# Kernel optimization log

Hardware: AMD Instinct MI355X
Metric: run time of the kernel (lower is better)

## Reference

```python
import jax, jax.numpy as jnp
from jax import lax
import numpy as np

NT, NGRID, NX = 365, 3000, 20
H, NY = 256, 1


def setup_inputs() -> dict:
    key = jax.random.key(0)
    ks = jax.random.split(key, 12)
    x = jax.random.normal(ks[0], (NT, NGRID, NX), dtype=jnp.float32)
    y = jax.random.normal(ks[1], (NT, NGRID, NY), dtype=jnp.float32)
    obs_mask = jax.random.bernoulli(ks[2], 0.7, (NT, NGRID, NY))
    y = jnp.where(obs_mask, y, jnp.nan)
    s_in = 1.0 / np.sqrt(NX + 1)
    s_h = 1.0 / np.sqrt(H)
    w_in = jax.random.uniform(ks[3], (H, NX + 1), jnp.float32, -s_in, s_in)
    b_in = jax.random.uniform(ks[4], (H,), jnp.float32, -s_in, s_in)
    w_ih = jax.random.uniform(ks[5], (4 * H, H), jnp.float32, -s_h, s_h)
    b_ih = jax.random.uniform(ks[6], (4 * H,), jnp.float32, -s_h, s_h)
    w_hh = jax.random.uniform(ks[7], (4 * H, H), jnp.float32, -s_h, s_h)
    b_hh = jax.random.uniform(ks[8], (4 * H,), jnp.float32, -s_h, s_h)
    w_out = jax.random.uniform(ks[9], (NY, H), jnp.float32, -s_h, s_h)
    b_out = jax.random.uniform(ks[10], (NY,), jnp.float32, -s_h, s_h)
    return {"x": x, "y": y, "w_in": w_in, "b_in": b_in, "w_ih": w_ih,
            "b_ih": b_ih, "w_hh": w_hh, "b_hh": b_hh, "w_out": w_out,
            "b_out": b_out}


def reference(x, y, w_in, b_in, w_ih, b_ih, w_hh, b_hh, w_out, b_out):
    nt, ngrid, nx = x.shape
    h0 = jnp.zeros((ngrid, H), x.dtype)
    c0 = jnp.zeros((ngrid, H), x.dtype)
    y0 = jnp.zeros((ngrid, NY), x.dtype)

    def step(carry, inp):
        h, c, yt = carry
        xt, yobs = inp                      # [ngrid,nx], [ngrid,ny]
        mask = ~jnp.isnan(yobs)
        yt = jnp.where(mask, yobs, yt)      # fill observed values
        xcat = jnp.concatenate([xt, yt], axis=1)          # [ngrid, nx+1]
        x0 = jax.nn.relu(xcat @ w_in.T + b_in)            # [ngrid, H]
        gates = x0 @ w_ih.T + b_ih + h @ w_hh.T + b_hh    # [ngrid, 4H]
        i, f, g, o = jnp.split(gates, 4, axis=1)
        c = jax.nn.sigmoid(f) * c + jax.nn.sigmoid(i) * jnp.tanh(g)
        h = jax.nn.sigmoid(o) * jnp.tanh(c)
        yt_new = h @ w_out.T + b_out                      # [ngrid, ny]
        return (h, c, yt_new), yt_new

    _, out = lax.scan(step, (h0, c0, y0), (x, y))
    return out  # [nt, ngrid, ny]
```

## Files before the change

kernel.cpp:

```cpp
#include <hip/hip_runtime.h>
#include <math.h>

#define NT     365
#define NGRID  3000
#define NX     20
#define H      256
#define CPB    15
#define NBLK   (NGRID/CPB)
#define THREADS 1024

#define WPK_US   (16*16*4*64*8)
#define WPKIN_US (16*2*64*8)

typedef short v8s __attribute__((ext_vector_type(8)));
typedef float v4f __attribute__((ext_vector_type(4)));
#define MFMA_BF16 __builtin_amdgcn_mfma_f32_16x16x32_bf16

__device__ __forceinline__ unsigned short f2bf(float f) {
    unsigned int u = __float_as_uint(f);
    u += 0x7fffu + ((u >> 16) & 1u);
    return (unsigned short)(u >> 16);
}
__device__ __forceinline__ float bf2f(unsigned short h) {
    return __uint_as_float(((unsigned int)h) << 16);
}
__device__ __forceinline__ float sigm(float x)  { return 1.0f / (1.0f + __expf(-x)); }
__device__ __forceinline__ float tanh_f(float x){ return 2.0f * sigm(2.0f * x) - 1.0f; }

__global__ void prep_kernel(const float* __restrict__ w_in,
                            const float* __restrict__ w_ih,
                            const float* __restrict__ w_hh,
                            const float* __restrict__ b_ih,
                            const float* __restrict__ b_hh,
                            unsigned short* __restrict__ wpk,
                            unsigned short* __restrict__ wpkin,
                            float* __restrict__ bsum) {
    int idx = blockIdx.x * 256 + threadIdx.x;
    if (idx < WPK_US) {
        int e    = idx & 7;
        int lane = (idx >> 3) & 63;
        int q    = (idx >> 9) & 3;
        int gk   = idx >> 11;
        int kap  = gk & 15, g = gk >> 4;
        int k = kap * 32 + ((lane >> 4) << 3) + e;
        int j = q * 256 + g * 16 + (lane & 15);
        float wv = (k < 256) ? w_ih[j * 256 + k] : w_hh[j * 256 + (k - 256)];
        wpk[idx] = f2bf(wv);
    }
    if (idx < WPKIN_US) {
        int e    = idx & 7;
        int lane = (idx >> 3) & 63;
        int d    = (idx >> 9) & 1;
        int tau  = idx >> 10;
        int k = ((lane >> 4) << 3) + e;
        int n = tau * 16 + (lane & 15);
        float wv = (k < NX + 1) ? w_in[n * (NX + 1) + k] : 0.0f;
        unsigned short hi = f2bf(wv);
        wpkin[idx] = d ? f2bf(wv - bf2f(hi)) : hi;
    }
    if (idx < 4 * H) bsum[idx] = b_ih[idx] + b_hh[idx];
}

__global__ __attribute__((amdgpu_flat_work_group_size(THREADS, THREADS),
                          amdgpu_waves_per_eu(4, 4)))
void lstm_main(const float* __restrict__ x,
               const float* __restrict__ y,
               const float* __restrict__ b_in,
               const float* __restrict__ w_out,
               const float* __restrict__ b_out,
               const unsigned short* __restrict__ wpk,
               const unsigned short* __restrict__ wpkin,
               const float* __restrict__ bsum,
               float* __restrict__ out) {
    __shared__ __align__(16) unsigned short Agh[16][512];
    __shared__ __align__(16) unsigned short Agl[16][512];
    __shared__ __align__(16) unsigned short Xh[512];
    __shared__ __align__(16) unsigned short Xl[512];
    __shared__ float y_part[16][16];
    __shared__ float lds_pad[12288];

    const int tid  = threadIdx.x;
    const int w    = tid >> 6;
    const int lane = tid & 63;
    const int col  = lane & 15;
    const int quad = lane >> 4;
    const int g0   = blockIdx.x * CPB;

    const int   jh   = w * 16 + col;
    const float b_i  = bsum[jh];
    const float b_f  = bsum[256 + jh];
    const float b_g  = bsum[512 + jh];
    const float b_o  = bsum[768 + jh];
    const float wo   = w_out[jh];
    const float bi_x = b_in[jh];
    const float bout = b_out[0];
    const int   kq_x = jh >> 5;
    const int   kq_h = 8 + (jh >> 5);
    const int   qp_w = (jh >> 3) & 3;
    const int   e_w  = jh & 7;
    const unsigned short* bbase = wpk + (size_t)(w * 16) * 4 * 512 + lane * 8;
    const unsigned short* bx_hi = wpkin + (w * 2 + 0) * 512 + lane * 8;
    const unsigned short* bx_lo = wpkin + (w * 2 + 1) * 512 + lane * 8;

    if (bout == -1234567.25f) {
        lds_pad[tid] = (float)tid;
        lds_pad[tid + 4096] = 1.f;
        lds_pad[tid + 8192] = 2.f;
    }

    {
        unsigned int* p;
        p = (unsigned int*)&Agh[0][0];
        for (int i = tid; i < 16 * 256; i += THREADS) p[i] = 0u;
        p = (unsigned int*)&Agl[0][0];
        for (int i = tid; i < 16 * 256; i += THREADS) p[i] = 0u;
        if (tid < 256) ((unsigned int*)&Xh[0])[tid] = 0u;
        if (tid < 256) ((unsigned int*)&Xl[0])[tid] = 0u;
    }
    float c_st[4];
    #pragma unroll
    for (int r = 0; r < 4; ++r) c_st[r] = 0.0f;
    __syncthreads();

    for (int t = 0; t < NT; ++t) {
        {
            const float* xr = x + ((size_t)t * NGRID + g0) * NX;
            if (tid < CPB * NX) {
                float v  = xr[tid];
                int cell = tid / NX;
                int k    = tid - cell * NX;
                int pos  = (((k >> 3) << 4) + cell) * 8 + (k & 7);
                unsigned short hi = f2bf(v);
                Xh[pos] = hi;
                Xl[pos] = f2bf(v - bf2f(hi));
            }
            if (tid < CPB) {
                float yo = y[(size_t)t * NGRID + g0 + tid];
                if (!__builtin_isnan(yo)) {
                    int pos = (2 * 16 + tid) * 8 + 4;
                    unsigned short hi = f2bf(yo);
                    Xh[pos] = hi;
                    Xl[pos] = f2bf(yo - bf2f(hi));
                }
            }
        }
        __syncthreads();

        {
            v8s bh  = *(const v8s*)bx_hi;
            v8s bl  = *(const v8s*)bx_lo;
            v8s xah = *(const v8s*)&Xh[lane * 8];
            v8s xal = *(const v8s*)&Xl[lane * 8];
            v4f acc = {0.0f, 0.0f, 0.0f, 0.0f};
            acc = MFMA_BF16(xah, bh, acc, 0, 0, 0);
            acc = MFMA_BF16(xah, bl, acc, 0, 0, 0);
            acc = MFMA_BF16(xal, bh, acc, 0, 0, 0);
            #pragma unroll
            for (int r = 0; r < 4; ++r) {
                int cell = quad * 4 + r;
                if (cell < CPB) {
                    float v = fmaxf(acc[r] + bi_x, 0.0f);
                    unsigned short hi = f2bf(v);
                    int pos = (qp_w * 16 + cell) * 8 + e_w;
                    Agh[kq_x][pos] = hi;
                    Agl[kq_x][pos] = f2bf(v - bf2f(hi));
                }
            }
        }
        __syncthreads();

        v4f acc[4];
        #pragma unroll
        for (int q = 0; q < 4; ++q) acc[q] = (v4f){0, 0, 0, 0};

        #pragma unroll 1
        for (int kap = 0; kap < 16; ++kap) {
            const unsigned short* bp = bbase + (size_t)kap * 4 * 512;
            v8s B[4];
            #pragma unroll
            for (int c = 0; c < 4; ++c)
                B[c] = *(const v8s*)(bp + c * 512);
            v8s Ah = *(const v8s*)&Agh[kap][lane * 8];
            v8s Al = *(const v8s*)&Agl[kap][lane * 8];
            #pragma unroll
            for (int q = 0; q < 4; ++q) {
                acc[q] = MFMA_BF16(Ah, B[q], acc[q], 0, 0, 0);
                acc[q] = MFMA_BF16(Al, B[q], acc[q], 0, 0, 0);
            }
        }
        __syncthreads();

        {
            float yp[4];
            #pragma unroll
            for (int r = 0; r < 4; ++r) {
                int cell = quad * 4 + r;
                float iv = acc[0][r] + b_i;
                float fv = acc[1][r] + b_f;
                float gv = acc[2][r] + b_g;
                float ov = acc[3][r] + b_o;
                float c  = fmaf(sigm(fv), c_st[r], sigm(iv) * tanh_f(gv));
                c_st[r]  = c;
                float h  = sigm(ov) * tanh_f(c);
                yp[r] = 0.0f;
                if (cell < CPB) {
                    unsigned short hi = f2bf(h);
                    int pos = (qp_w * 16 + cell) * 8 + e_w;
                    Agh[kq_h][pos] = hi;
                    Agl[kq_h][pos] = f2bf(h - bf2f(hi));
                    yp[r] = h * wo;
                }
            }
            #pragma unroll
            for (int r = 0; r < 4; ++r) {
                float p = yp[r];
                p += __shfl_xor(p, 1);
                p += __shfl_xor(p, 2);
                p += __shfl_xor(p, 4);
                p += __shfl_xor(p, 8);
                if (col == 0)
                    y_part[w][quad * 4 + r] = p;
            }
        }
        __syncthreads();

        if (tid < CPB) {
            float yv = bout;
            #pragma unroll
            for (int w2 = 0; w2 < 16; ++w2) yv += y_part[w2][tid];
            out[(size_t)t * NGRID + g0 + tid] = yv;
            int pos = (2 * 16 + tid) * 8 + 4;
            unsigned short hi = f2bf(yv);
            Xh[pos] = hi;
            Xl[pos] = f2bf(yv - bf2f(hi));
        }
    }

    if (bout == -1234567.25f)
        out[tid & 3] += lds_pad[tid] + lds_pad[tid + 4096] + lds_pad[tid + 8192];
}

extern "C" void kernel_launch(void* const* d_in, const int* in_sizes, int n_in,
                              void* d_out, int out_size, void* d_ws, size_t ws_size,
                              hipStream_t stream) {
    const float* x     = (const float*)d_in[0];
    const float* y     = (const float*)d_in[1];
    const float* w_in  = (const float*)d_in[2];
    const float* b_in  = (const float*)d_in[3];
    const float* w_ih  = (const float*)d_in[4];
    const float* b_ih  = (const float*)d_in[5];
    const float* w_hh  = (const float*)d_in[6];
    const float* b_hh  = (const float*)d_in[7];
    const float* w_out = (const float*)d_in[8];
    const float* b_out = (const float*)d_in[9];

    unsigned short* wpk   = (unsigned short*)d_ws;
    unsigned short* wpkin = wpk + WPK_US;
    float*          bsum  = (float*)(wpkin + WPKIN_US);
    float*          out   = (float*)d_out;

    prep_kernel<<<(WPK_US + 255) / 256, 256, 0, stream>>>(
        w_in, w_ih, w_hh, b_ih, b_hh, wpk, wpkin, bsum);
    lstm_main<<<NBLK, THREADS, 0, stream>>>(
        x, y, b_in, w_out, b_out, wpk, wpkin, bsum, out);
}
```

Before: 4.446 ms.

## Reorder recurrent GEMM around barriers, keep weight slices in registers, prefetch inputs

Removes the barrier between the input projection and the gate GEMM. The K-slices are reordered so that slices 8–15 are accumulated before the next barrier and slices 0–7 after it. Three weight K-slices stay resident in registers for the whole kernel, a fourth is prefetched after each barrier, and the input-layer weights are hoisted out of the time loop. Next-step x/y values are loaded into registers during the current step so global latency overlaps compute. The cost is higher register pressure, and correctness depends on which waves write which LDS slices before they are read without a barrier.

```diff
diff --git a/kernel.cpp b/kernel.cpp
--- a/kernel.cpp
+++ b/kernel.cpp
@@ -11,6 +11,9 @@
 
 #define WPK_US   (16*16*4*64*8)
 #define WPKIN_US (16*2*64*8)
+
+#define KPERS 3
+#define KPRE  11
 
 typedef short v8s __attribute__((ext_vector_type(8)));
 typedef float v4f __attribute__((ext_vector_type(4)));
@@ -117,49 +120,63 @@
         if (tid < 256) ((unsigned int*)&Xh[0])[tid] = 0u;
         if (tid < 256) ((unsigned int*)&Xl[0])[tid] = 0u;
     }
+
+    v8s Bp[KPERS][4];
+    #pragma unroll
+    for (int kp = 0; kp < KPERS; ++kp) {
+        #pragma unroll
+        for (int c2 = 0; c2 < 4; ++c2)
+            Bp[kp][c2] = *(const v8s*)(bbase + ((size_t)(8 + kp) * 4 + c2) * 512);
+    }
+    v8s Bpre[4];
+    #pragma unroll
+    for (int c2 = 0; c2 < 4; ++c2)
+        Bpre[c2] = *(const v8s*)(bbase + ((size_t)KPRE * 4 + c2) * 512);
+
+    const v8s bxh = *(const v8s*)bx_hi;
+    const v8s bxl = *(const v8s*)bx_lo;
+
+    float xv = 0.0f, yv = 0.0f;
+    if (tid < CPB * NX) xv = x[(size_t)g0 * NX + tid];
+    if (tid < CPB)      yv = y[(size_t)g0 + tid];
+
     float c_st[4];
     #pragma unroll
     for (int r = 0; r < 4; ++r) c_st[r] = 0.0f;
     __syncthreads();
 
     for (int t = 0; t < NT; ++t) {
+        if (tid < CPB * NX) {
+            float v  = xv;
+            int cell = tid / NX;
+            int k    = tid - cell * NX;
+            int pos  = (((k >> 3) << 4) + cell) * 8 + (k & 7);
+            unsigned short hi = f2bf(v);
+            Xh[pos] = hi;
+            Xl[pos] = f2bf(v - bf2f(hi));
+        }
+        if (tid < CPB) {
+            if (!__builtin_isnan(yv)) {
+                int pos = (2 * 16 + tid) * 8 + 4;
+                unsigned short hi = f2bf(yv);
+                Xh[pos] = hi;
+                Xl[pos] = f2bf(yv - bf2f(hi));
+            }
+        }
+        __syncthreads();
+
         {
-            const float* xr = x + ((size_t)t * NGRID + g0) * NX;
-            if (tid < CPB * NX) {
-                float v  = xr[tid];
-                int cell = tid / NX;
-                int k    = tid - cell * NX;
-                int pos  = (((k >> 3) << 4) + cell) * 8 + (k & 7);
-                unsigned short hi = f2bf(v);
-                Xh[pos] = hi;
-                Xl[pos] = f2bf(v - bf2f(hi));
-            }
-            if (tid < CPB) {
-                float yo = y[(size_t)t * NGRID + g0 + tid];
-                if (!__builtin_isnan(yo)) {
-                    int pos = (2 * 16 + tid) * 8 + 4;
-                    unsigned short hi = f2bf(yo);
-                    Xh[pos] = hi;
-                    Xl[pos] = f2bf(yo - bf2f(hi));
-                }
-            }
-        }
-        __syncthreads();
-
-        {
-            v8s bh  = *(const v8s*)bx_hi;
-            v8s bl  = *(const v8s*)bx_lo;
             v8s xah = *(const v8s*)&Xh[lane * 8];
             v8s xal = *(const v8s*)&Xl[lane * 8];
-            v4f acc = {0.0f, 0.0f, 0.0f, 0.0f};
-            acc = MFMA_BF16(xah, bh, acc, 0, 0, 0);
-            acc = MFMA_BF16(xah, bl, acc, 0, 0, 0);
-            acc = MFMA_BF16(xal, bh, acc, 0, 0, 0);
+            v4f xacc = {0.0f, 0.0f, 0.0f, 0.0f};
+            xacc = MFMA_BF16(xah, bxh, xacc, 0, 0, 0);
+            xacc = MFMA_BF16(xah, bxl, xacc, 0, 0, 0);
+            xacc = MFMA_BF16(xal, bxh, xacc, 0, 0, 0);
             #pragma unroll
             for (int r = 0; r < 4; ++r) {
                 int cell = quad * 4 + r;
                 if (cell < CPB) {
-                    float v = fmaxf(acc[r] + bi_x, 0.0f);
+                    float v = fmaxf(xacc[r] + bi_x, 0.0f);
                     unsigned short hi = f2bf(v);
                     int pos = (qp_w * 16 + cell) * 8 + e_w;
                     Agh[kq_x][pos] = hi;
@@ -167,19 +184,37 @@
                 }
             }
         }
-        __syncthreads();
 
         v4f acc[4];
         #pragma unroll
-        for (int q = 0; q < 4; ++q) acc[q] = (v4f){0, 0, 0, 0};
-
+        for (int q = 0; q < 4; ++q) acc[q] = (v4f){0.0f, 0.0f, 0.0f, 0.0f};
+
+        #pragma unroll
+        for (int kp = 0; kp < KPERS; ++kp) {
+            v8s Ah = *(const v8s*)&Agh[8 + kp][lane * 8];
+            v8s Al = *(const v8s*)&Agl[8 + kp][lane * 8];
+            #pragma unroll
+            for (int q = 0; q < 4; ++q) {
+                acc[q] = MFMA_BF16(Ah, Bp[kp][q], acc[q], 0, 0, 0);
+                acc[q] = MFMA_BF16(Al, Bp[kp][q], acc[q], 0, 0, 0);
+            }
+        }
+        {
+            v8s Ah = *(const v8s*)&Agh[KPRE][lane * 8];
+            v8s Al = *(const v8s*)&Agl[KPRE][lane * 8];
+            #pragma unroll
+            for (int q = 0; q < 4; ++q) {
+                acc[q] = MFMA_BF16(Ah, Bpre[q], acc[q], 0, 0, 0);
+                acc[q] = MFMA_BF16(Al, Bpre[q], acc[q], 0, 0, 0);
+            }
+        }
         #pragma unroll 1
-        for (int kap = 0; kap < 16; ++kap) {
+        for (int kap = 12; kap < 16; ++kap) {
             const unsigned short* bp = bbase + (size_t)kap * 4 * 512;
             v8s B[4];
             #pragma unroll
-            for (int c = 0; c < 4; ++c)
-                B[c] = *(const v8s*)(bp + c * 512);
+            for (int c2 = 0; c2 < 4; ++c2)
+                B[c2] = *(const v8s*)(bp + c2 * 512);
             v8s Ah = *(const v8s*)&Agh[kap][lane * 8];
             v8s Al = *(const v8s*)&Agl[kap][lane * 8];
             #pragma unroll
@@ -189,6 +224,30 @@
             }
         }
         __syncthreads();
+
+        {
+            const int tn = (t + 1 < NT) ? (t + 1) : t;
+            if (tid < CPB * NX)
+                xv = x[((size_t)tn * NGRID + g0) * NX + tid];
+            if (tid < CPB)
+                yv = y[(size_t)tn * NGRID + g0 + tid];
+        }
+
+        #pragma unroll 1
+        for (int kap = 0; kap < 8; ++kap) {
+            const unsigned short* bp = bbase + (size_t)kap * 4 * 512;
+            v8s B[4];
+            #pragma unroll
+            for (int c2 = 0; c2 < 4; ++c2)
+                B[c2] = *(const v8s*)(bp + c2 * 512);
+            v8s Ah = *(const v8s*)&Agh[kap][lane * 8];
+            v8s Al = *(const v8s*)&Agl[kap][lane * 8];
+            #pragma unroll
+            for (int q = 0; q < 4; ++q) {
+                acc[q] = MFMA_BF16(Ah, B[q], acc[q], 0, 0, 0);
+                acc[q] = MFMA_BF16(Al, B[q], acc[q], 0, 0, 0);
+            }
+        }
 
         {
             float yp[4];
@@ -224,15 +283,19 @@
         }
         __syncthreads();
 
+        #pragma unroll
+        for (int c2 = 0; c2 < 4; ++c2)
+            Bpre[c2] = *(const v8s*)(bbase + ((size_t)KPRE * 4 + c2) * 512);
+
         if (tid < CPB) {
-            float yv = bout;
-            #pragma unroll
-            for (int w2 = 0; w2 < 16; ++w2) yv += y_part[w2][tid];
-            out[(size_t)t * NGRID + g0 + tid] = yv;
+            float yfin = bout;
+            #pragma unroll
+            for (int w2 = 0; w2 < 16; ++w2) yfin += y_part[w2][tid];
+            out[(size_t)t * NGRID + g0 + tid] = yfin;
             int pos = (2 * 16 + tid) * 8 + 4;
-            unsigned short hi = f2bf(yv);
+            unsigned short hi = f2bf(yfin);
             Xh[pos] = hi;
-            Xl[pos] = f2bf(yv - bf2f(hi));
+            Xl[pos] = f2bf(yfin - bf2f(hi));
         }
     }
 
```

After: 4.977 ms. 12.0% more time.
